# Kernel tuning notes

Hardware: AMD Instinct MI355X
Metric: run time of the kernel (lower is better)

Reference implementation:

```python
import jax, jax.numpy as jnp
import numpy as np

B, C, H, W = 16, 3, 128, 128
PATCH = 8
E = 512          # embedding_dim
NH = 8           # num_heads
P = 64           # proj_dim
HID = 2048       # hidden_dim
L = 6            # num_layers
COND = 3
PH, PW = H // PATCH, W // PATCH
S = PH * PW + 1  # sequence length (patches + cond token)
INV_SQRT_E = 1.0 / np.float32(np.sqrt(E))

_PARAM_SHAPES = {
    'patch_w': (E, C, PATCH, PATCH), 'patch_b': (E,),
    'cond_w1': (COND, E), 'cond_b1': (E,), 'cond_w2': (E, E), 'cond_b2': (E,),
    'pos_embed': (1, S, E),
    'enc_vp': (L, NH, E, P), 'enc_kp': (L, NH, E, P), 'enc_qh': (L, NH, S, S), 'enc_lift': (L, 1, NH * P, E),
    'enc_ln1g': (L, E), 'enc_ln1b': (L, E),
    'enc_w1': (L, E, HID), 'enc_b1': (L, HID), 'enc_w2': (L, HID, E), 'enc_b2': (L, E),
    'enc_ln2g': (L, E), 'enc_ln2b': (L, E),
    'dec_vp': (L, NH, E, P), 'dec_kp': (L, NH, E, P), 'dec_qh': (L, NH, S, S), 'dec_lift': (L, 1, NH * P, E),
    'dec_ln2g': (L, E), 'dec_ln2b': (L, E),
    'dec_w1': (L, E, HID), 'dec_b1': (L, HID), 'dec_w2': (L, HID, E), 'dec_b2': (L, E),
    'dec_ln3g': (L, E), 'dec_ln3b': (L, E),
    'final_g': (E,), 'final_b': (E,),
    'deconv_w': (E, C, PATCH, PATCH), 'deconv_b': (C,),
}


def setup_inputs() -> dict:
    key = jax.random.key(0)
    inp = {
        'x': jax.random.normal(jax.random.fold_in(key, 1000), (B, C, H, W), jnp.float32),
        'y': jax.random.normal(jax.random.fold_in(key, 1001), (B, COND), jnp.float32),
    }
    for i, (name, shp) in enumerate(_PARAM_SHAPES.items()):
        w = 0.02 * jax.random.normal(jax.random.fold_in(key, i), shp, jnp.float32)
        if name.endswith('g'):  # layernorm gains near 1
            w = w + 1.0
        inp[name] = w
    return inp


def _ln(x, g, b, eps=1e-5):
    m = x.mean(-1, keepdims=True)
    v = ((x - m) ** 2).mean(-1, keepdims=True)
    return (x - m) * jax.lax.rsqrt(v + eps) * g + b


def _mhsa(x, vp, kp, qh, lift):
    # x: (B,S,E); vp/kp: (NH,E,P); qh: (NH,S,S); lift: (1, NH*P, E)
    k = jnp.einsum('bse,hep->bhsp', x, kp)
    v = jnp.einsum('bse,hep->bhsp', x, vp)
    qv = jnp.einsum('hst,bhtp->bhsp', qh, v)
    # a_ts = (qh@V) @ K^T, then transpose(-2,-1): a[t,s] = qv[s] . k[t]
    a = jnp.einsum('bhsp,bhtp->bhts', qv, k) * INV_SQRT_E
    a = jax.nn.softmax(a, axis=-1)
    o = jnp.einsum('bhst,bhtp->bhsp', a, v)          # (B,NH,S,P)
    o = o.transpose(0, 2, 1, 3).reshape(x.shape[0], S, NH * P)
    return o @ lift[0]


def _block(z, vp, kp, qh, lift, g1, b1, w1, fb1, w2, fb2, g2, b2):
    z = _ln(z + _mhsa(z, vp, kp, qh, lift), g1, b1)
    h = jax.nn.leaky_relu(z @ w1 + fb1, 0.2) @ w2 + fb2  # dropout = identity (eval)
    return _ln(z + h, g2, b2)


def reference(x, y, patch_w, patch_b, cond_w1, cond_b1, cond_w2, cond_b2, pos_embed,
              enc_vp, enc_kp, enc_qh, enc_lift, enc_ln1g, enc_ln1b,
              enc_w1, enc_b1, enc_w2, enc_b2, enc_ln2g, enc_ln2b,
              dec_vp, dec_kp, dec_qh, dec_lift, dec_ln2g, dec_ln2b,
              dec_w1, dec_b1, dec_w2, dec_b2, dec_ln3g, dec_ln3b,
              final_g, final_b, deconv_w, deconv_b):
    b = x.shape[0]
    # Patching: Conv2d(k=p, s=p) == block-reshape + einsum
    xp = x.reshape(b, C, PH, PATCH, PW, PATCH)
    tok = jnp.einsum('bchpwq,ecpq->bhwe', xp, patch_w).reshape(b, PH * PW, E) + patch_b
    cond = jax.nn.leaky_relu(y @ cond_w1 + cond_b1, 0.2)
    cond = jax.nn.leaky_relu(cond @ cond_w2 + cond_b2, 0.2)
    z = jnp.concatenate([cond[:, None, :], tok], axis=1) + pos_embed
    for i in range(L):
        z = _block(z, enc_vp[i], enc_kp[i], enc_qh[i], enc_lift[i],
                   enc_ln1g[i], enc_ln1b[i], enc_w1[i], enc_b1[i],
                   enc_w2[i], enc_b2[i], enc_ln2g[i], enc_ln2b[i])
    for i in range(L):  # decoder: only mhsa_2 / ln2 / ff / ln3 are used
        z = _block(z, dec_vp[i], dec_kp[i], dec_qh[i], dec_lift[i],
                   dec_ln2g[i], dec_ln2b[i], dec_w1[i], dec_b1[i],
                   dec_w2[i], dec_b2[i], dec_ln3g[i], dec_ln3b[i])
    z = _ln(z[:, 1:], final_g, final_b)               # drop cond token
    g = z.reshape(b, PH, PW, E)                        # (B,E,PH,PW) grid, channels-last form
    out = jnp.einsum('bhwe,ecpq->bchpwq', g, deconv_w).reshape(b, C, H, W)
    return out + deconv_b[None, :, None, None]
```

## Files before the change

kernel.cpp:

```cpp
#include <hip/hip_runtime.h>
#include <stdint.h>
#include <math.h>

#define B_    16
#define C_    3
#define HIMG  128
#define E_    512
#define NH_   8
#define S_    257
#define T_    256
#define MTOK  4096
#define MSEQ  4112
#define HID_  2048
#define SP_   288
#define SLAB  (288*288)
#define INV_SQRT_E 0.044194173824159216f

typedef __attribute__((ext_vector_type(8))) __bf16 bf16x8;
typedef __attribute__((ext_vector_type(4))) float f32x4;

__device__ __forceinline__ void gload16(const void* g, const void* lds)
{
    __builtin_amdgcn_global_load_lds(
        (const __attribute__((address_space(1))) uint32_t*)(uintptr_t)g,
        (__attribute__((address_space(3))) uint32_t*)(uint32_t)(uintptr_t)lds,
        16, 0, 0);
}

template<int WMW, int WNW, bool LEAKY, bool OUTF32>
__device__ __forceinline__ void gemm_core(
    const __bf16* __restrict__ A, int lda,
    const __bf16* __restrict__ Bt, int ldb,
    void* __restrict__ C, int ldc,
    const float* __restrict__ bias, float scale,
    int M, int N, int K, int tm, int tn)
{
    constexpr int BM = WMW * 64;
    constexpr int BN = WNW * 32;
    constexpr int T  = WMW * WNW * 64;
    constexpr int AC = BM * 4;
    constexpr int BC = BN * 4;
    __shared__ __align__(16) __bf16 sA[2][BM * 32];
    __shared__ __align__(16) __bf16 sB[2][BN * 32];

    const int tid  = threadIdx.x;
    const int lane = tid & 63;
    const int wid  = tid >> 6;
    const int wm   = wid / WNW;
    const int wn   = wid % WNW;
    const int lh   = lane >> 4;
    const int ll   = lane & 15;

    const __bf16* Ab = A + (long)tm * BM * lda;
    const __bf16* Bb = Bt + (long)tn * BN * ldb;

    f32x4 acc[4][2] = {};
    const int nst = K >> 5;

    auto stage = [&](int buf, int k0) {
#pragma unroll
        for (int rr = 0; rr < AC / T; ++rr) {
            const int L = rr * T + tid;
            const int row = L >> 2;
            const int gch = (L & 3) ^ ((row >> 1) & 3);
            gload16(Ab + (long)row * lda + k0 + gch * 8,
                    (const char*)(&sA[buf][0]) + (rr * T + (wid << 6)) * 16);
        }
#pragma unroll
        for (int rr = 0; rr < BC / T; ++rr) {
            const int L = rr * T + tid;
            const int row = L >> 2;
            const int gch = (L & 3) ^ ((row >> 1) & 3);
            gload16(Bb + (long)row * ldb + k0 + gch * 8,
                    (const char*)(&sB[buf][0]) + (rr * T + (wid << 6)) * 16);
        }
    };

    stage(0, 0);
    __syncthreads();
    for (int st = 0; st < nst; ++st) {
        const int cur = st & 1;
        if (st + 1 < nst) stage(cur ^ 1, (st + 1) << 5);

        bf16x8 afr[4], bfr[2];
#pragma unroll
        for (int i = 0; i < 4; ++i) {
            const int rw = wm * 64 + i * 16 + ll;
            const int c  = lh ^ ((rw >> 1) & 3);
            afr[i] = *reinterpret_cast<const bf16x8*>(&sA[cur][rw * 32 + c * 8]);
        }
#pragma unroll
        for (int j = 0; j < 2; ++j) {
            const int rw = wn * 32 + j * 16 + ll;
            const int c  = lh ^ ((rw >> 1) & 3);
            bfr[j] = *reinterpret_cast<const bf16x8*>(&sB[cur][rw * 32 + c * 8]);
        }
#pragma unroll
        for (int i = 0; i < 4; ++i)
#pragma unroll
            for (int j = 0; j < 2; ++j)
                acc[i][j] = __builtin_amdgcn_mfma_f32_16x16x32_bf16(
                                afr[i], bfr[j], acc[i][j], 0, 0, 0);
        if (st + 1 < nst) __syncthreads();
    }

#pragma unroll
    for (int i = 0; i < 4; ++i)
#pragma unroll
        for (int ii = 0; ii < 4; ++ii) {
            const int m = tm * BM + wm * 64 + i * 16 + lh * 4 + ii;
            if (m >= M) continue;
#pragma unroll
            for (int j = 0; j < 2; ++j) {
                const int n = tn * BN + wn * 32 + j * 16 + ll;
                if (n >= N) continue;
                float v = acc[i][j][ii] * scale;
                if (bias) v += bias[n];
                if (LEAKY) v = v > 0.f ? v : 0.2f * v;
                if (OUTF32) ((float*)C)[(long)m * ldc + n] = v;
                else        ((__bf16*)C)[(long)m * ldc + n] = (__bf16)v;
            }
        }
}

template<int WMW, int WNW, bool LEAKY, bool OUTF32>
__global__ __launch_bounds__(WMW * WNW * 64) void gemm_k(
    const __bf16* __restrict__ A, int lda, const __bf16* __restrict__ Bt, int ldb,
    void* __restrict__ C, int ldc, const float* __restrict__ bias, float scale,
    int M, int N, int K, int ntn)
{
    const int nwg = gridDim.x;
    int wg = blockIdx.x;
    const int q = nwg >> 3, r = nwg & 7;
    if (q > 0) {
        const int xcd = wg & 7, off = wg >> 3;
        wg = (xcd < r ? xcd * (q + 1) : r * (q + 1) + (xcd - r) * q) + off;
    }
    gemm_core<WMW, WNW, LEAKY, OUTF32>(A, lda, Bt, ldb, C, ldc, bias, scale,
                                       M, N, K, wg / ntn, wg % ntn);
}

__global__ __launch_bounds__(256) void qv_k(const __bf16* __restrict__ qhb,
                                            const __bf16* __restrict__ vT,
                                            __bf16* __restrict__ qvcat)
{
    const int bh = blockIdx.z, b = bh >> 3, h = bh & 7;
    gemm_core<2, 2, false, false>(qhb + (long)h * SLAB, SP_,
                                  vT + (long)bh * 64 * SP_, SP_,
                                  qvcat + (long)b * S_ * E_ + h * 64, E_,
                                  nullptr, 1.f, S_, 64, SP_, blockIdx.x, 0);
}

__global__ __launch_bounds__(256) void scores_k(const __bf16* __restrict__ kvcat,
                                                const __bf16* __restrict__ qvcat,
                                                __bf16* __restrict__ attnb)
{
    const int bh = blockIdx.z, b = bh >> 3, h = bh & 7;
    gemm_core<2, 2, false, false>(kvcat + (long)b * S_ * 1024 + h * 64, 1024,
                                  qvcat + (long)b * S_ * E_ + h * 64, E_,
                                  attnb + (long)bh * SLAB, SP_,
                                  nullptr, INV_SQRT_E, S_, S_, 64,
                                  blockIdx.x, blockIdx.y);
}

__global__ __launch_bounds__(256) void av_k(const __bf16* __restrict__ attnb,
                                            const __bf16* __restrict__ vT,
                                            __bf16* __restrict__ ocat)
{
    const int bh = blockIdx.z, b = bh >> 3, h = bh & 7;
    gemm_core<2, 2, false, false>(attnb + (long)bh * SLAB, SP_,
                                  vT + (long)bh * 64 * SP_, SP_,
                                  ocat + (long)b * S_ * E_ + h * 64, E_,
                                  nullptr, 1.f, S_, 64, SP_, blockIdx.x, 0);
}

__global__ void softmax_kernel(__bf16* __restrict__ attnb)
{
    const int rowid = blockIdx.x * 4 + (threadIdx.x >> 6);
    const int lane  = threadIdx.x & 63;
    const int bh = rowid / S_, s = rowid % S_;
    __bf16* p = attnb + (long)bh * SLAB + (long)s * SP_;
    const float v0 = (float)p[lane],       v1 = (float)p[lane + 64];
    const float v2 = (float)p[lane + 128], v3 = (float)p[lane + 192];
    const float vx = (lane == 0) ? (float)p[256] : -1e30f;
    float m = fmaxf(fmaxf(fmaxf(v0, v1), fmaxf(v2, v3)), vx);
#pragma unroll
    for (int o = 32; o; o >>= 1) m = fmaxf(m, __shfl_xor(m, o));
    const float e0 = __expf(v0 - m), e1 = __expf(v1 - m);
    const float e2 = __expf(v2 - m), e3 = __expf(v3 - m);
    const float ex = (lane == 0) ? __expf(vx - m) : 0.f;
    float su = e0 + e1 + e2 + e3 + ex;
#pragma unroll
    for (int o = 32; o; o >>= 1) su += __shfl_xor(su, o);
    const float inv = 1.f / su;
    p[lane]       = (__bf16)(e0 * inv);
    p[lane + 64]  = (__bf16)(e1 * inv);
    p[lane + 128] = (__bf16)(e2 * inv);
    p[lane + 192] = (__bf16)(e3 * inv);
    if (lane == 0) p[256] = (__bf16)(ex * inv);
    if (lane >= 1 && lane < 32) p[256 + lane] = (__bf16)0.f;
}

__global__ void ln_kernel(const float* __restrict__ x, const float* __restrict__ r,
                          const float* __restrict__ g, const float* __restrict__ bb,
                          float* __restrict__ outf, __bf16* __restrict__ outb,
                          int skip_cond, int nrows)
{
    const int row = blockIdx.x * 4 + (threadIdx.x >> 6);
    if (row >= nrows) return;
    const int lane = threadIdx.x & 63;
    const long xrow = skip_cond ? (long)row + (row >> 8) + 1 : (long)row;
    const float4* xr = (const float4*)(x + xrow * E_) + lane * 2;
    float4 a = xr[0], b4 = xr[1];
    if (r) {
        const float4* rr = (const float4*)(r + (long)row * E_) + lane * 2;
        const float4 c = rr[0], d = rr[1];
        a.x += c.x; a.y += c.y; a.z += c.z; a.w += c.w;
        b4.x += d.x; b4.y += d.y; b4.z += d.z; b4.w += d.w;
    }
    float e[8] = {a.x, a.y, a.z, a.w, b4.x, b4.y, b4.z, b4.w};
    float s = 0.f;
#pragma unroll
    for (int i = 0; i < 8; ++i) s += e[i];
#pragma unroll
    for (int o = 32; o; o >>= 1) s += __shfl_xor(s, o);
    const float mean = s * (1.f / 512.f);
    float v = 0.f;
#pragma unroll
    for (int i = 0; i < 8; ++i) { e[i] -= mean; v += e[i] * e[i]; }
#pragma unroll
    for (int o = 32; o; o >>= 1) v += __shfl_xor(v, o);
    const float inv = rsqrtf(v * (1.f / 512.f) + 1e-5f);
    const float4* gp = (const float4*)g + lane * 2;
    const float4* bp = (const float4*)bb + lane * 2;
    const float4 g0 = gp[0], g1 = gp[1], bb0 = bp[0], bb1 = bp[1];
    const float gv[8] = {g0.x, g0.y, g0.z, g0.w, g1.x, g1.y, g1.z, g1.w};
    const float bv[8] = {bb0.x, bb0.y, bb0.z, bb0.w, bb1.x, bb1.y, bb1.z, bb1.w};
    float o8[8];
#pragma unroll
    for (int i = 0; i < 8; ++i) o8[i] = e[i] * inv * gv[i] + bv[i];
    if (outf) {
        float4* of = (float4*)(outf + (long)row * E_) + lane * 2;
        of[0] = make_float4(o8[0], o8[1], o8[2], o8[3]);
        of[1] = make_float4(o8[4], o8[5], o8[6], o8[7]);
    }
    if (outb) {
        bf16x8 ov;
#pragma unroll
        for (int i = 0; i < 8; ++i) ov[i] = (__bf16)o8[i];
        *reinterpret_cast<bf16x8*>(outb + (long)row * E_ + lane * 8) = ov;
    }
}

__global__ void conv_straight(const float* __restrict__ in, __bf16* __restrict__ out, long n)
{
    const long i = (long)blockIdx.x * 256 + threadIdx.x;
    if (i < n) out[i] = (__bf16)in[i];
}

__global__ void conv_transpose(const float* __restrict__ in, __bf16* __restrict__ out,
                               int R, int C, long in_bs, long out_bs)
{
    __shared__ float tile[32][33];
    const int bt = blockIdx.z;
    const float* ip = in + (long)bt * in_bs;
    __bf16* op = out + (long)bt * out_bs;
    const int r0 = blockIdx.x * 32, c0 = blockIdx.y * 32;
    const int tx = threadIdx.x & 31, ty = threadIdx.x >> 5;
#pragma unroll
    for (int i = 0; i < 32; i += 8) {
        const int rr = r0 + ty + i, cc = c0 + tx;
        tile[ty + i][tx] = (rr < R && cc < C) ? ip[(long)rr * C + cc] : 0.f;
    }
    __syncthreads();
#pragma unroll
    for (int i = 0; i < 32; i += 8) {
        const int cc = c0 + ty + i, rr = r0 + tx;
        if (cc < C && rr < R) op[(long)cc * R + rr] = (__bf16)tile[tx][ty + i];
    }
}

__global__ void wconv_kernel(const float* __restrict__ kp, const float* __restrict__ vp,
                             const float* __restrict__ lift, const float* __restrict__ w1,
                             const float* __restrict__ w2,
                             __bf16* __restrict__ kvT, __bf16* __restrict__ liftT,
                             __bf16* __restrict__ w1T, __bf16* __restrict__ w2T)
{
    const int j = blockIdx.y;
    const float* src; __bf16* dst; int R, C, nb;
    switch (j) {
        case 0:  src = kp;   dst = kvT;          R = 512;  C = 64;   nb = 8; break;
        case 1:  src = vp;   dst = kvT + 262144; R = 512;  C = 64;   nb = 8; break;
        case 2:  src = lift; dst = liftT;        R = 512;  C = 512;  nb = 1; break;
        case 3:  src = w1;   dst = w1T;          R = 512;  C = 2048; nb = 1; break;
        default: src = w2;   dst = w2T;          R = 2048; C = 512;  nb = 1; break;
    }
    const int tR = R >> 5, tC = C >> 5;
    int t = blockIdx.x;
    if (t >= tR * tC * nb) return;
    const int bt = t / (tR * tC);
    t %= tR * tC;
    const int rt = t / tC, ct = t % tC;
    const long bs = (long)R * C;
    const float* ip = src + (long)bt * bs;
    __bf16* op = dst + (long)bt * bs;
    __shared__ float tile[32][33];
    const int tx = threadIdx.x & 31, ty = threadIdx.x >> 5;
#pragma unroll
    for (int i = 0; i < 32; i += 8)
        tile[ty + i][tx] = ip[(long)(rt * 32 + ty + i) * C + ct * 32 + tx];
    __syncthreads();
#pragma unroll
    for (int i = 0; i < 32; i += 8)
        op[(long)(ct * 32 + ty + i) * R + rt * 32 + tx] = (__bf16)tile[tx][ty + i];
}

__global__ void conv_qh(const float* __restrict__ qh, __bf16* __restrict__ out)
{
    const long n = 8L * SLAB;
    for (long o = (long)blockIdx.x * 256 + threadIdx.x; o < n; o += (long)gridDim.x * 256) {
        const int t = (int)(o % SP_);
        const long rr = o / SP_;
        const int s = (int)(rr % SP_);
        const int h = (int)(rr / SP_);
        float v = 0.f;
        if (s < S_ && t < S_) v = qh[((long)h * S_ + s) * S_ + t];
        out[o] = (__bf16)v;
    }
}

__global__ void vtrans_kernel(const __bf16* __restrict__ kvcat, __bf16* __restrict__ vT)
{
    __shared__ __bf16 tile[32][33];
    const int bh = blockIdx.z, b = bh >> 3, h = bh & 7;
    const int t0 = blockIdx.x * 32, p0 = blockIdx.y * 32;
    const int tx = threadIdx.x & 31, ty = threadIdx.x >> 5;
#pragma unroll
    for (int i = 0; i < 32; i += 8) {
        const int t = t0 + ty + i;
        tile[ty + i][tx] = (t < S_) ?
            kvcat[((long)(b * S_ + t)) * 1024 + 512 + h * 64 + p0 + tx] : (__bf16)0.f;
    }
    __syncthreads();
#pragma unroll
    for (int i = 0; i < 32; i += 8)
        vT[(long)bh * 64 * SP_ + (long)(p0 + ty + i) * SP_ + t0 + tx] = tile[tx][ty + i];
}

__global__ void im2col_kernel(const float* __restrict__ x, __bf16* __restrict__ xcol)
{
    const int idx = blockIdx.x * 256 + threadIdx.x;
    if (idx >= MTOK * 192) return;
    const int m = idx / 192, k = idx % 192;
    const int b = m >> 8, t = m & 255;
    const int ph = t >> 4, pw = t & 15;
    const int c = k >> 6, rr = k & 63;
    const int p = rr >> 3, q = rr & 7;
    xcol[idx] = (__bf16)x[(((long)(b * C_ + c) * HIMG) + ph * 8 + p) * HIMG + pw * 8 + q];
}

__global__ void cond_kernel(const float* __restrict__ y,
                            const float* __restrict__ w1, const float* __restrict__ b1,
                            const float* __restrict__ w2, const float* __restrict__ b2,
                            const float* __restrict__ pos,
                            float* __restrict__ z, __bf16* __restrict__ zb)
{
    __shared__ float c1[512];
    const int b = blockIdx.x;
    const int e = threadIdx.x;
    float v = y[b * 3 + 0] * w1[e] + y[b * 3 + 1] * w1[512 + e]
            + y[b * 3 + 2] * w1[1024 + e] + b1[e];
    v = v > 0.f ? v : 0.2f * v;
    c1[e] = v;
    __syncthreads();
    float acc = b2[e];
    for (int k = 0; k < 512; ++k) acc += c1[k] * w2[k * 512 + e];
    acc = acc > 0.f ? acc : 0.2f * acc;
    const float o = acc + pos[e];
    z[(long)b * S_ * E_ + e] = o;
    zb[(long)b * S_ * E_ + e] = (__bf16)o;
}

__global__ void assemble_kernel(const float* __restrict__ tok,
                                const float* __restrict__ pos,
                                float* __restrict__ z, __bf16* __restrict__ zb)
{
    const int idx = blockIdx.x * 256 + threadIdx.x;
    if (idx >= MTOK * E_) return;
    const int m = idx >> 9;
    const int e = idx & 511;
    const int b = m >> 8, t = m & 255;
    const float o = tok[idx] + pos[(1 + t) * E_ + e];
    const long zi = ((long)b * S_ + 1 + t) * E_ + e;
    z[zi] = o;
    zb[zi] = (__bf16)o;
}

__global__ void scatter_kernel(const float* __restrict__ dtmp,
                               const float* __restrict__ db,
                               float* __restrict__ out)
{
    const int idx = blockIdx.x * 256 + threadIdx.x;
    if (idx >= B_ * C_ * HIMG * HIMG) return;
    const int b  = idx / (C_ * HIMG * HIMG);
    const int rm = idx % (C_ * HIMG * HIMG);
    const int c  = rm / (HIMG * HIMG);
    const int hh = (rm % (HIMG * HIMG)) / HIMG;
    const int ww = rm % HIMG;
    const int ph = hh >> 3, p = hh & 7;
    const int pw = ww >> 3, q = ww & 7;
    out[idx] = dtmp[((long)(b * 256 + ph * 16 + pw)) * 192 + c * 64 + p * 8 + q] + db[c];
}

extern "C" void kernel_launch(void* const* d_in, const int* in_sizes, int n_in,
                              void* d_out, int out_size, void* d_ws, size_t ws_size,
                              hipStream_t stream)
{
    const float* x        = (const float*)d_in[0];
    const float* y        = (const float*)d_in[1];
    const float* patch_w  = (const float*)d_in[2];
    const float* patch_b  = (const float*)d_in[3];
    const float* cond_w1  = (const float*)d_in[4];
    const float* cond_b1  = (const float*)d_in[5];
    const float* cond_w2  = (const float*)d_in[6];
    const float* cond_b2  = (const float*)d_in[7];
    const float* pos      = (const float*)d_in[8];
    const float* enc_vp   = (const float*)d_in[9];
    const float* enc_kp   = (const float*)d_in[10];
    const float* enc_qh   = (const float*)d_in[11];
    const float* enc_lift = (const float*)d_in[12];
    const float* enc_ln1g = (const float*)d_in[13];
    const float* enc_ln1b = (const float*)d_in[14];
    const float* enc_w1   = (const float*)d_in[15];
    const float* enc_b1   = (const float*)d_in[16];
    const float* enc_w2   = (const float*)d_in[17];
    const float* enc_b2   = (const float*)d_in[18];
    const float* enc_ln2g = (const float*)d_in[19];
    const float* enc_ln2b = (const float*)d_in[20];
    const float* dec_vp   = (const float*)d_in[21];
    const float* dec_kp   = (const float*)d_in[22];
    const float* dec_qh   = (const float*)d_in[23];
    const float* dec_lift = (const float*)d_in[24];
    const float* dec_ln2g = (const float*)d_in[25];
    const float* dec_ln2b = (const float*)d_in[26];
    const float* dec_w1   = (const float*)d_in[27];
    const float* dec_b1   = (const float*)d_in[28];
    const float* dec_w2   = (const float*)d_in[29];
    const float* dec_b2   = (const float*)d_in[30];
    const float* dec_ln3g = (const float*)d_in[31];
    const float* dec_ln3b = (const float*)d_in[32];
    const float* final_g  = (const float*)d_in[33];
    const float* final_b  = (const float*)d_in[34];
    const float* deconv_w = (const float*)d_in[35];
    const float* deconv_b = (const float*)d_in[36];
    float* out = (float*)d_out;

    char* wp = (char*)d_ws;
    auto alloc_f32 = [&](long n) { float* p = (float*)wp; wp += ((n * 4 + 63) & ~63LL); return p; };
    auto alloc_bf  = [&](long n) { __bf16* p = (__bf16*)wp; wp += ((n * 2 + 63) & ~63LL); return p; };

    float*  z      = alloc_f32(2105344);
    float*  tok    = alloc_f32(2097152);
    float*  res    = alloc_f32(2105344);
    float*  dtmp   = alloc_f32(786432);
    __bf16* zb     = alloc_bf(4352L * 512);
    __bf16* xcolb  = alloc_bf(786432);
    __bf16* kvcat  = alloc_bf(4352L * 1024);
    __bf16* qvcat  = alloc_bf(4352L * 512);
    __bf16* ocat   = alloc_bf(4352L * 512);
    __bf16* vT     = alloc_bf(128L * 64 * SP_);
    __bf16* attnb  = alloc_bf(128L * SLAB + 96L * SP_);
    __bf16* hidden = alloc_bf(4224L * 2048);
    __bf16* gbuf   = alloc_bf(4096L * 512);
    __bf16* pwb    = alloc_bf(512L * 192);
    __bf16* dwTb   = alloc_bf(192L * 512);
    __bf16* kvTb   = alloc_bf(1024L * 512);
    __bf16* liftTb = alloc_bf(262144);
    __bf16* w1Tb   = alloc_bf(1048576);
    __bf16* w2Tb   = alloc_bf(1048576);
    __bf16* qhb    = alloc_bf(8L * SLAB + 96L * SP_);
    (void)ws_size; (void)in_sizes; (void)n_in; (void)out_size;

    const dim3 blk(256);

    conv_straight<<<dim3(384), blk, 0, stream>>>(patch_w, pwb, 98304);
    conv_transpose<<<dim3(16, 6, 1), blk, 0, stream>>>(deconv_w, dwTb, 512, 192, 0, 0);

    im2col_kernel<<<dim3(3072), blk, 0, stream>>>(x, xcolb);
    gemm_k<2, 2, false, true><<<dim3(256), blk, 0, stream>>>(
        xcolb, 192, pwb, 192, tok, 512, patch_b, 1.f, MTOK, 512, 192, 8);
    cond_kernel<<<dim3(B_), dim3(512), 0, stream>>>(y, cond_w1, cond_b1,
                                                    cond_w2, cond_b2, pos, z, zb);
    assemble_kernel<<<dim3(8192), blk, 0, stream>>>(tok, pos, z, zb);

    for (int l = 0; l < 12; ++l) {
        const bool enc = l < 6;
        const int  li  = enc ? l : l - 6;
        const float* vp   = (enc ? enc_vp   : dec_vp)   + (long)li * NH_ * E_ * 64;
        const float* kp   = (enc ? enc_kp   : dec_kp)   + (long)li * NH_ * E_ * 64;
        const float* qh   = (enc ? enc_qh   : dec_qh)   + (long)li * NH_ * S_ * S_;
        const float* lift = (enc ? enc_lift : dec_lift) + (long)li * 512 * 512;
        const float* g1   = (enc ? enc_ln1g : dec_ln2g) + li * E_;
        const float* bb1  = (enc ? enc_ln1b : dec_ln2b) + li * E_;
        const float* w1   = (enc ? enc_w1   : dec_w1)   + (long)li * E_ * HID_;
        const float* fb1  = (enc ? enc_b1   : dec_b1)   + li * HID_;
        const float* w2   = (enc ? enc_w2   : dec_w2)   + (long)li * HID_ * E_;
        const float* fb2  = (enc ? enc_b2   : dec_b2)   + li * E_;
        const float* g2   = (enc ? enc_ln2g : dec_ln3g) + li * E_;
        const float* bb2  = (enc ? enc_ln2b : dec_ln3b) + li * E_;

        wconv_kernel<<<dim3(1024, 5), blk, 0, stream>>>(kp, vp, lift, w1, w2,
                                                        kvTb, liftTb, w1Tb, w2Tb);
        conv_qh<<<dim3(2592), blk, 0, stream>>>(qh, qhb);

        gemm_k<2, 4, false, false><<<dim3(264), dim3(512), 0, stream>>>(
            zb, 512, kvTb, 512, kvcat, 1024, nullptr, 1.f, MSEQ, 1024, 512, 8);
        vtrans_kernel<<<dim3(9, 2, 128), blk, 0, stream>>>(kvcat, vT);
        qv_k<<<dim3(3, 1, 128), blk, 0, stream>>>(qhb, vT, qvcat);
        scores_k<<<dim3(3, 5, 128), blk, 0, stream>>>(kvcat, qvcat, attnb);
        softmax_kernel<<<dim3(8224), blk, 0, stream>>>(attnb);
        av_k<<<dim3(3, 1, 128), blk, 0, stream>>>(attnb, vT, ocat);
        gemm_k<2, 2, false, true><<<dim3(264), blk, 0, stream>>>(
            ocat, 512, liftTb, 512, res, 512, nullptr, 1.f, MSEQ, 512, 512, 8);
        ln_kernel<<<dim3(1028), blk, 0, stream>>>(z, res, g1, bb1, z, zb, 0, MSEQ);

        gemm_k<2, 4, true, false><<<dim3(528), dim3(512), 0, stream>>>(
            zb, 512, w1Tb, 512, hidden, 2048, fb1, 1.f, MSEQ, HID_, 512, 16);
        gemm_k<2, 2, false, true><<<dim3(264), blk, 0, stream>>>(
            hidden, 2048, w2Tb, 2048, res, 512, fb2, 1.f, MSEQ, 512, HID_, 8);
        ln_kernel<<<dim3(1028), blk, 0, stream>>>(z, res, g2, bb2, z, zb, 0, MSEQ);
    }

    ln_kernel<<<dim3(1024), blk, 0, stream>>>(z, nullptr, final_g, final_b,
                                              nullptr, gbuf, 1, MTOK);
    gemm_k<2, 2, false, true><<<dim3(96), blk, 0, stream>>>(
        gbuf, 512, dwTb, 512, dtmp, 192, nullptr, 1.f, MTOK, 192, 512, 3);
    scatter_kernel<<<dim3(3072), blk, 0, stream>>>(dtmp, deconv_b, out);
}
```

Before: 1.766 ms.

## Deepen GEMM prefetch pipeline and split-K the N=512 projection GEMMs

The shared GEMM core moves from a double buffer to a four-stage LDS ring with three tiles in flight, using explicit vmcnt waits and a single barrier per k-step in place of two __syncthreads. The lift and FFN2 GEMMs, which have N=512 and only 264 workgroups, are split along K into 2 and 4 parts that write bf16 partials into the reused attention buffer. The LayerNorm kernel then sums those partials, replacing the fp32 residual buffer. This raises occupancy and hides global-load latency, at the cost of more LDS per block, extra partial traffic, and bf16 rounding of each partial sum.

```diff
diff --git a/kernel.cpp b/kernel.cpp
--- a/kernel.cpp
+++ b/kernel.cpp
@@ -14,6 +14,7 @@
 #define HID_  2048
 #define SP_   288
 #define SLAB  (288*288)
+#define PS    2105344L
 #define INV_SQRT_E 0.044194173824159216f
 
 typedef __attribute__((ext_vector_type(8))) __bf16 bf16x8;
@@ -35,13 +36,14 @@
     const float* __restrict__ bias, float scale,
     int M, int N, int K, int tm, int tn)
 {
-    constexpr int BM = WMW * 64;
-    constexpr int BN = WNW * 32;
-    constexpr int T  = WMW * WNW * 64;
-    constexpr int AC = BM * 4;
-    constexpr int BC = BN * 4;
-    __shared__ __align__(16) __bf16 sA[2][BM * 32];
-    __shared__ __align__(16) __bf16 sB[2][BN * 32];
+    constexpr int BM  = WMW * 64;
+    constexpr int BN  = WNW * 32;
+    constexpr int T   = WMW * WNW * 64;
+    constexpr int ACH = BM * 4;
+    constexpr int BCH = BN * 4;
+    constexpr int LPT = ACH / T + BCH / T;
+    __shared__ __align__(16) __bf16 sA[4][BM * 32];
+    __shared__ __align__(16) __bf16 sB[4][BN * 32];
 
     const int tid  = threadIdx.x;
     const int lane = tid & 63;
@@ -59,7 +61,7 @@
 
     auto stage = [&](int buf, int k0) {
 #pragma unroll
-        for (int rr = 0; rr < AC / T; ++rr) {
+        for (int rr = 0; rr < ACH / T; ++rr) {
             const int L = rr * T + tid;
             const int row = L >> 2;
             const int gch = (L & 3) ^ ((row >> 1) & 3);
@@ -67,7 +69,7 @@
                     (const char*)(&sA[buf][0]) + (rr * T + (wid << 6)) * 16);
         }
 #pragma unroll
-        for (int rr = 0; rr < BC / T; ++rr) {
+        for (int rr = 0; rr < BCH / T; ++rr) {
             const int L = rr * T + tid;
             const int row = L >> 2;
             const int gch = (L & 3) ^ ((row >> 1) & 3);
@@ -76,12 +78,20 @@
         }
     };
 
-    stage(0, 0);
-    __syncthreads();
+    const int PF = nst < 3 ? nst : 3;
+    for (int s = 0; s < PF; ++s) stage(s & 3, s << 5);
+
     for (int st = 0; st < nst; ++st) {
-        const int cur = st & 1;
-        if (st + 1 < nst) stage(cur ^ 1, (st + 1) << 5);
-
+        const int rem = nst - 1 - st;
+        if (rem >= 2)      asm volatile("s_waitcnt vmcnt(%0)" :: "n"(2 * LPT) : "memory");
+        else if (rem == 1) asm volatile("s_waitcnt vmcnt(%0)" :: "n"(LPT) : "memory");
+        else               asm volatile("s_waitcnt vmcnt(0)" ::: "memory");
+        __builtin_amdgcn_s_barrier();
+        __builtin_amdgcn_sched_barrier(0);
+
+        if (st + 3 < nst) stage((st + 3) & 3, (st + 3) << 5);
+
+        const int cur = st & 3;
         bf16x8 afr[4], bfr[2];
 #pragma unroll
         for (int i = 0; i < 4; ++i) {
@@ -101,7 +111,6 @@
             for (int j = 0; j < 2; ++j)
                 acc[i][j] = __builtin_amdgcn_mfma_f32_16x16x32_bf16(
                                 afr[i], bfr[j], acc[i][j], 0, 0, 0);
-        if (st + 1 < nst) __syncthreads();
     }
 
 #pragma unroll
@@ -123,21 +132,39 @@
         }
 }
 
+__device__ __forceinline__ int xcd_swizzle(int wg, int nwg)
+{
+    const int q = nwg >> 3, r = nwg & 7;
+    if (q == 0) return wg;
+    const int xcd = wg & 7, off = wg >> 3;
+    return (xcd < r ? xcd * (q + 1) : r * (q + 1) + (xcd - r) * q) + off;
+}
+
 template<int WMW, int WNW, bool LEAKY, bool OUTF32>
 __global__ __launch_bounds__(WMW * WNW * 64) void gemm_k(
     const __bf16* __restrict__ A, int lda, const __bf16* __restrict__ Bt, int ldb,
     void* __restrict__ C, int ldc, const float* __restrict__ bias, float scale,
     int M, int N, int K, int ntn)
 {
-    const int nwg = gridDim.x;
-    int wg = blockIdx.x;
-    const int q = nwg >> 3, r = nwg & 7;
-    if (q > 0) {
-        const int xcd = wg & 7, off = wg >> 3;
-        wg = (xcd < r ? xcd * (q + 1) : r * (q + 1) + (xcd - r) * q) + off;
-    }
+    const int wg = xcd_swizzle(blockIdx.x, gridDim.x);
     gemm_core<WMW, WNW, LEAKY, OUTF32>(A, lda, Bt, ldb, C, ldc, bias, scale,
                                        M, N, K, wg / ntn, wg % ntn);
+}
+
+template<int WMW, int WNW>
+__global__ __launch_bounds__(WMW * WNW * 64) void gemm_split_k(
+    const __bf16* __restrict__ A, int lda, const __bf16* __restrict__ Bt, int ldb,
+    __bf16* __restrict__ P, long pstride, const float* __restrict__ bias,
+    int M, int N, int K, int npart, int ntn)
+{
+    const int part = blockIdx.y;
+    const int Kp = K / npart;
+    const int wg = xcd_swizzle(blockIdx.x, gridDim.x);
+    gemm_core<WMW, WNW, false, false>(A + (long)part * Kp, lda,
+                                      Bt + (long)part * Kp, ldb,
+                                      P + (long)part * pstride, N,
+                                      part == 0 ? bias : nullptr, 1.f,
+                                      M, N, Kp, wg / ntn, wg % ntn);
 }
 
 __global__ __launch_bounds__(256) void qv_k(const __bf16* __restrict__ qhb,
@@ -201,7 +228,8 @@
     if (lane >= 1 && lane < 32) p[256 + lane] = (__bf16)0.f;
 }
 
-__global__ void ln_kernel(const float* __restrict__ x, const float* __restrict__ r,
+__global__ void ln_kernel(const float* __restrict__ x,
+                          const __bf16* __restrict__ parts, int nparts, long pstride,
                           const float* __restrict__ g, const float* __restrict__ bb,
                           float* __restrict__ outf, __bf16* __restrict__ outb,
                           int skip_cond, int nrows)
@@ -211,14 +239,14 @@
     const int lane = threadIdx.x & 63;
     const long xrow = skip_cond ? (long)row + (row >> 8) + 1 : (long)row;
     const float4* xr = (const float4*)(x + xrow * E_) + lane * 2;
-    float4 a = xr[0], b4 = xr[1];
-    if (r) {
-        const float4* rr = (const float4*)(r + (long)row * E_) + lane * 2;
-        const float4 c = rr[0], d = rr[1];
-        a.x += c.x; a.y += c.y; a.z += c.z; a.w += c.w;
-        b4.x += d.x; b4.y += d.y; b4.z += d.z; b4.w += d.w;
-    }
+    const float4 a = xr[0], b4 = xr[1];
     float e[8] = {a.x, a.y, a.z, a.w, b4.x, b4.y, b4.z, b4.w};
+    for (int p = 0; p < nparts; ++p) {
+        const bf16x8 pv = *reinterpret_cast<const bf16x8*>(
+            parts + (long)p * pstride + (long)row * E_ + lane * 8);
+#pragma unroll
+        for (int i = 0; i < 8; ++i) e[i] += (float)pv[i];
+    }
     float s = 0.f;
 #pragma unroll
     for (int i = 0; i < 8; ++i) s += e[i];
@@ -461,7 +489,6 @@
 
     float*  z      = alloc_f32(2105344);
     float*  tok    = alloc_f32(2097152);
-    float*  res    = alloc_f32(2105344);
     float*  dtmp   = alloc_f32(786432);
     __bf16* zb     = alloc_bf(4352L * 512);
     __bf16* xcolb  = alloc_bf(786432);
@@ -520,18 +547,20 @@
         scores_k<<<dim3(3, 5, 128), blk, 0, stream>>>(kvcat, qvcat, attnb);
         softmax_kernel<<<dim3(8224), blk, 0, stream>>>(attnb);
         av_k<<<dim3(3, 1, 128), blk, 0, stream>>>(attnb, vT, ocat);
-        gemm_k<2, 2, false, true><<<dim3(264), blk, 0, stream>>>(
-            ocat, 512, liftTb, 512, res, 512, nullptr, 1.f, MSEQ, 512, 512, 8);
-        ln_kernel<<<dim3(1028), blk, 0, stream>>>(z, res, g1, bb1, z, zb, 0, MSEQ);
+        gemm_split_k<2, 2><<<dim3(264, 2), blk, 0, stream>>>(
+            ocat, 512, liftTb, 512, attnb, PS, nullptr, MSEQ, 512, 512, 2, 8);
+        ln_kernel<<<dim3(1028), blk, 0, stream>>>(z, attnb, 2, PS, g1, bb1,
+                                                  z, zb, 0, MSEQ);
 
         gemm_k<2, 4, true, false><<<dim3(528), dim3(512), 0, stream>>>(
             zb, 512, w1Tb, 512, hidden, 2048, fb1, 1.f, MSEQ, HID_, 512, 16);
-        gemm_k<2, 2, false, true><<<dim3(264), blk, 0, stream>>>(
-            hidden, 2048, w2Tb, 2048, res, 512, fb2, 1.f, MSEQ, 512, HID_, 8);
-        ln_kernel<<<dim3(1028), blk, 0, stream>>>(z, res, g2, bb2, z, zb, 0, MSEQ);
-    }
-
-    ln_kernel<<<dim3(1024), blk, 0, stream>>>(z, nullptr, final_g, final_b,
+        gemm_split_k<2, 2><<<dim3(264, 4), blk, 0, stream>>>(
+            hidden, 2048, w2Tb, 2048, attnb, PS, fb2, MSEQ, 512, HID_, 4, 8);
+        ln_kernel<<<dim3(1028), blk, 0, stream>>>(z, attnb, 4, PS, g2, bb2,
+                                                  z, zb, 0, MSEQ);
+    }
+
+    ln_kernel<<<dim3(1024), blk, 0, stream>>>(z, nullptr, 0, 0, final_g, final_b,
                                               nullptr, gbuf, 1, MTOK);
     gemm_k<2, 2, false, true><<<dim3(96), blk, 0, stream>>>(
         gbuf, 512, dwTb, 512, dtmp, 192, nullptr, 1.f, MTOK, 192, 512, 3);
```

Measured after the change: 1.770 ms. No clear change (+0.2%).
